# Kernel tuning notes

Measured on AMD Instinct MI355X. Metric: run time of the kernel, lower is better.

The kernel has to match this reference:

```python
import jax, jax.numpy as jnp
import numpy as np

N, E, IN, H, L = 50000, 640000, 64, 128, 3
EPS_DIST = 1e-8
LN_EPS = 1e-5


def setup_inputs() -> dict:
    key = jax.random.key(0)
    ks = iter(jax.random.split(key, 64))

    def rn(shape, fan_in):
        return (jax.random.normal(next(ks), shape, jnp.float32) / np.sqrt(fan_in)).astype(jnp.float32)

    inp = {}
    inp['h'] = jax.random.normal(next(ks), (N, IN), jnp.float32)
    inp['x'] = jax.random.normal(next(ks), (N, 3), jnp.float32)
    inp['edge_index'] = jax.random.randint(next(ks), (2, E), 0, N, jnp.int64)
    # embedding_in: Linear(IN, H)
    inp['W_emb'] = rn((IN, H), IN); inp['b_emb'] = jnp.zeros((H,), jnp.float32)
    # per-layer EquivariantConv params, stacked over L
    inp['Wm1'] = rn((L, 2 * H + 1, H), 2 * H + 1); inp['bm1'] = jnp.zeros((L, H), jnp.float32)
    inp['Wm2'] = rn((L, H, H), H);                 inp['bm2'] = jnp.zeros((L, H), jnp.float32)
    inp['Wc1'] = rn((L, H, H), H);                 inp['bc1'] = jnp.zeros((L, H), jnp.float32)
    inp['Wc2'] = rn((L, H, 1), H)  # no bias
    inp['Wn1'] = rn((L, 2 * H, H), 2 * H);         inp['bn1'] = jnp.zeros((L, H), jnp.float32)
    inp['Wn2'] = rn((L, H, H), H);                 inp['bn2'] = jnp.zeros((L, H), jnp.float32)
    inp['ln_g'] = jnp.ones((L, H), jnp.float32);   inp['ln_b'] = jnp.zeros((L, H), jnp.float32)
    # epsilon head params
    inp['Wem1'] = rn((2 * H + 4, H), 2 * H + 4);   inp['bem1'] = jnp.zeros((H,), jnp.float32)
    inp['Wem2'] = rn((H, H), H);                   inp['bem2'] = jnp.zeros((H,), jnp.float32)
    inp['Wec1'] = rn((H, H), H);                   inp['bec1'] = jnp.zeros((H,), jnp.float32)
    inp['Wec2'] = rn((H, 3), H);                   inp['bec2'] = jnp.zeros((3,), jnp.float32)
    inp['Wh1'] = rn((H + 3, H), H + 3);            inp['bh1'] = jnp.zeros((H,), jnp.float32)
    inp['Wh2'] = rn((H, 3), H);                    inp['bh2'] = jnp.zeros((3,), jnp.float32)
    return inp


def _layernorm(v, g, b):
    mu = jnp.mean(v, axis=-1, keepdims=True)
    var = jnp.mean((v - mu) ** 2, axis=-1, keepdims=True)
    return (v - mu) * jax.lax.rsqrt(var + LN_EPS) * g + b


def reference(h, x, edge_index, W_emb, b_emb, Wm1, bm1, Wm2, bm2, Wc1, bc1, Wc2,
              Wn1, bn1, Wn2, bn2, ln_g, ln_b, Wem1, bem1, Wem2, bem2,
              Wec1, bec1, Wec2, bec2, Wh1, bh1, Wh2, bh2):
    row, col = edge_index[0], edge_index[1]
    n = x.shape[0]
    seg = lambda v: jax.ops.segment_sum(v, col, num_segments=n)
    in_degree = seg(jnp.ones((col.shape[0], 1), x.dtype))  # [N,1]

    h = h @ W_emb + b_emb  # embedding_in

    for i in range(L):
        rel = x[row] - x[col]                                   # [E,3]
        dist = jnp.linalg.norm(rel, axis=-1, keepdims=True)     # [E,1]
        mi = jnp.concatenate([h[row], h[col], dist], axis=-1)   # [E,2H+1]
        m = jax.nn.silu(jax.nn.silu(mi @ Wm1[i] + bm1[i]) @ Wm2[i] + bm2[i])
        agg = seg(m)                                            # [N,H]
        rel_dir = rel / (dist + EPS_DIST)
        coord_mult = jnp.tanh(jax.nn.silu(m @ Wc1[i] + bc1[i]) @ Wc2[i])  # [E,1]
        coord_update = seg(coord_mult * rel_dir)                # [N,3]
        x = x + coord_update / (in_degree + 1.0)
        nu = jnp.concatenate([h, agg], axis=-1)
        h = h + jax.nn.silu(nu @ Wn1[i] + bn1[i]) @ Wn2[i] + bn2[i]
        h = _layernorm(h, ln_g[i], ln_b[i])

    # predict_epsilon (eps_directional_head=False, eps_use_local_head=True, eps_normalize_agg=False)
    rel = x[row] - x[col]
    dist = jnp.linalg.norm(rel, axis=-1, keepdims=True)
    mi = jnp.concatenate([h[row], h[col], rel, dist], axis=-1)  # [E,2H+4]
    em = jax.nn.silu(jax.nn.silu(mi @ Wem1 + bem1) @ Wem2 + bem2)
    eps_src = jax.nn.silu(em @ Wec1 + bec1) @ Wec2 + bec2       # [E,3]
    eps = seg(eps_src)                                          # [N,3]
    hx = jnp.concatenate([h, x], axis=-1)
    eps = eps + jax.nn.silu(hx @ Wh1 + bh1) @ Wh2 + bh2
    return (h, x, eps)
```

## Files before the change

kernel.cpp:

```cpp
#include <hip/hip_runtime.h>

#define N_NODES 50000
#define N_EDGES 640000
#define HDIM    128
#define NLAYERS 3

typedef __attribute__((ext_vector_type(4))) float f32x4;
typedef short s16x8 __attribute__((ext_vector_type(8)));
typedef __bf16 bf16v8 __attribute__((ext_vector_type(8)));

static __device__ __forceinline__ unsigned short f2b(float f){
  unsigned int u = __float_as_uint(f);
  unsigned int r = u + 0x7FFFu + ((u >> 16) & 1u);
  return (unsigned short)(r >> 16);
}
static __device__ __forceinline__ float b2f(unsigned short h){
  return __uint_as_float(((unsigned int)h) << 16);
}
static __device__ __forceinline__ float silu_f(float x){
  return x / (1.0f + __expf(-x));
}
static __device__ __forceinline__ f32x4 MFMA(s16x8 a, s16x8 b, f32x4 c){
  return __builtin_amdgcn_mfma_f32_16x16x32_bf16(
      __builtin_bit_cast(bf16v8, a), __builtin_bit_cast(bf16v8, b), c, 0, 0, 0);
}

static __device__ __forceinline__ s16x8 ldA(const unsigned short* __restrict__ WT,
                                            int K, int s, int kk, int lane){
  const unsigned short* p = WT + (size_t)((s<<4) + (lane&15))*K + (kk<<5) + ((lane>>4)<<2);
  ushort4 a = *(const ushort4*)p;
  ushort4 b = *(const ushort4*)(p + 16);
  s16x8 r;
  r[0]=(short)a.x; r[1]=(short)a.y; r[2]=(short)a.z; r[3]=(short)a.w;
  r[4]=(short)b.x; r[5]=(short)b.y; r[6]=(short)b.z; r[7]=(short)b.w;
  return r;
}
static __device__ __forceinline__ s16x8 ldBf32(const float* __restrict__ p, int q){
  float4 a = *(const float4*)(p + (q<<2));
  float4 b = *(const float4*)(p + 16 + (q<<2));
  s16x8 r;
  r[0]=(short)f2b(a.x); r[1]=(short)f2b(a.y); r[2]=(short)f2b(a.z); r[3]=(short)f2b(a.w);
  r[4]=(short)f2b(b.x); r[5]=(short)f2b(b.y); r[6]=(short)f2b(b.z); r[7]=(short)f2b(b.w);
  return r;
}

#define STAGE(T) do { \
    const unsigned short* _src = blob + (((size_t)(T))<<12) + (w<<10) + (lane<<3); \
    unsigned char* _dst = &sm.wbuf[(T)&1][w<<11]; \
    __builtin_amdgcn_global_load_lds((const __attribute__((address_space(1))) void*)_src, \
        (__attribute__((address_space(3))) void*)_dst, 16, 0, 0); \
    __builtin_amdgcn_global_load_lds((const __attribute__((address_space(1))) void*)(_src+512), \
        (__attribute__((address_space(3))) void*)(_dst+1024), 16, 0, 0); \
  } while(0)
#define WAITV2 asm volatile("s_waitcnt vmcnt(2)" ::: "memory")
#define WAITV0 asm volatile("s_waitcnt vmcnt(0)" ::: "memory")
#define BARF do{ __builtin_amdgcn_s_barrier(); asm volatile("" ::: "memory"); }while(0)
#define EBAR do{ asm volatile("" ::: "memory"); __builtin_amdgcn_s_barrier(); }while(0)

__global__ void k_conv(const float* __restrict__ W, unsigned short* __restrict__ WT, int kshift){
  const int K = 1 << kshift;
  const int idx = (blockIdx.x<<8) + threadIdx.x;
  if (idx < (K<<7)){
    const int n = idx >> kshift;
    const int k = idx & (K-1);
    WT[idx] = f2b(W[(size_t)k*HDIM + n]);
  }
}

__global__ void k_conv_blob(const float* __restrict__ W1, const float* __restrict__ W2,
                            const float* __restrict__ W3, unsigned short* __restrict__ blob){
  const int i = (blockIdx.x<<8) + threadIdx.x;
  const int t = i >> 12;
  const int n = (i >> 5) & 127;
  const int slot = (i >> 3) & 3;
  const int j = i & 7;
  const int q = slot ^ ((n >> 1) & 3);
  const int kl = ((j >> 2) << 4) + (q << 2) + (j & 3);
  const float* W; int k;
  if (t < 8){ W = W1; k = (t<<5) + kl; }
  else if (t < 12){ W = W2; k = ((t-8)<<5) + kl; }
  else { W = W3; k = ((t-12)<<5) + kl; }
  blob[i] = f2b(W[(size_t)k*HDIM + n]);
}

__global__ void k_degree(const int* __restrict__ coli, int* __restrict__ degi){
  const int e = (blockIdx.x<<8) + threadIdx.x;
  if (e < N_EDGES) atomicAdd(&degi[coli[e]], 1);
}
__global__ void k_scanA(const int* __restrict__ degi, int* __restrict__ off, int* __restrict__ bsum){
  const int t = threadIdx.x, b = blockIdx.x;
  const int i = (b<<8) + t;
  const int v = (i < N_NODES) ? degi[i] : 0;
  int x = v;
  const int lane = t & 63;
  #pragma unroll
  for (int d=1; d<64; d<<=1){ int y = __shfl_up(x, d); if (lane >= d) x += y; }
  __shared__ int wsum[4];
  if (lane == 63) wsum[t>>6] = x;
  __syncthreads();
  int wo = 0;
  #pragma unroll
  for (int w=0; w<4; ++w) if (w < (t>>6)) wo += wsum[w];
  const int incl = x + wo;
  if (i < N_NODES) off[i] = incl - v;
  if (t == 255) bsum[b] = incl;
}
__global__ void k_scanB(int* __restrict__ bsum, int nb){
  const int t = threadIdx.x;
  const int v = (t < nb) ? bsum[t] : 0;
  int x = v;
  const int lane = t & 63;
  #pragma unroll
  for (int d=1; d<64; d<<=1){ int y = __shfl_up(x, d); if (lane >= d) x += y; }
  __shared__ int wsum[4];
  if (lane == 63) wsum[t>>6] = x;
  __syncthreads();
  int wo = 0;
  #pragma unroll
  for (int w=0; w<4; ++w) if (w < (t>>6)) wo += wsum[w];
  const int incl = x + wo;
  if (t < nb) bsum[t] = incl - v;
}
__global__ void k_scanC(int* __restrict__ off, const int* __restrict__ bsum, int* __restrict__ cursor){
  const int i = (blockIdx.x<<8) + threadIdx.x;
  if (i < N_NODES){
    const int o = off[i] + bsum[i>>8];
    off[i] = o;
    cursor[i] = o;
  }
}
__global__ void k_fill(const int* __restrict__ coli, int* __restrict__ cursor, int* __restrict__ elist){
  const int e = (blockIdx.x<<8) + threadIdx.x;
  if (e < N_EDGES){
    const int p = atomicAdd(&cursor[coli[e]], 1);
    elist[p] = e;
  }
}
__global__ void k_xcopy(const float* __restrict__ xin, float* __restrict__ xbuf){
  const int i = (blockIdx.x<<8) + threadIdx.x;
  if (i < N_NODES*3) xbuf[i] = xin[i];
}

__global__ __launch_bounds__(256) void k_embed(
    const float* __restrict__ hin, const unsigned short* __restrict__ WembT,
    const float* __restrict__ bemb, float* __restrict__ hbuf,
    unsigned short* __restrict__ hb)
{
  __shared__ float s_b[128];
  const int tid = threadIdx.x;
  if (tid < 128) s_b[tid] = bemb[tid];
  __syncthreads();
  const int lane = tid & 63, q = lane>>4;
  const int n = (blockIdx.x<<6) + ((tid>>6)<<4) + (lane&15);
  const bool valid = n < N_NODES;
  const int nc = valid ? n : (N_NODES-1);
  const float* __restrict__ hp = hin + (size_t)nc*64;
  f32x4 acc[8];
  #pragma unroll
  for (int s=0;s<8;++s)
    #pragma unroll
    for (int r=0;r<4;++r) acc[s][r] = s_b[(s<<4)+(q<<2)+r];
  #pragma unroll
  for (int kk=0;kk<2;++kk){
    const s16x8 bf = ldBf32(hp + (kk<<5), q);
    #pragma unroll
    for (int s=0;s<8;++s) acc[s] = MFMA(ldA(WembT, 64, s, kk, lane), bf, acc[s]);
  }
  if (valid){
    float* op = hbuf + (size_t)n*HDIM;
    unsigned short* hbw = hb + (size_t)n*HDIM;
    #pragma unroll
    for (int s=0;s<8;++s){
      float4 o; o.x=acc[s][0]; o.y=acc[s][1]; o.z=acc[s][2]; o.w=acc[s][3];
      *(float4*)(op + (s<<4) + (q<<2)) = o;
      ushort4 u; u.x=f2b(o.x); u.y=f2b(o.y); u.z=f2b(o.z); u.w=f2b(o.w);
      *(ushort4*)(hbw + ((s>>1)<<5) + (q<<3) + ((s&1)<<2)) = u;
    }
  }
}

template<bool CSR>
__global__ __launch_bounds__(256) void k_edge_mlp(
    const unsigned short* __restrict__ hb, const float* __restrict__ xbuf,
    const int* __restrict__ rowi, const int* __restrict__ coli,
    const unsigned short* __restrict__ blob,
    const float* __restrict__ bm1v, const float* __restrict__ wm1r256,
    const float* __restrict__ bm2v, const float* __restrict__ bc1v,
    const float* __restrict__ wc2v,
    unsigned short* __restrict__ m_buf, float* __restrict__ agg,
    float* __restrict__ cu)
{
  __shared__ struct {
    alignas(16) unsigned char wbuf[2][8192];
    int row[128]; int col[128];
    float dist[128]; float rdir[128][3];
    float b1[128], w256[128], b2[128], bc1[128], wc2[128];
  } sm;
  const int tid = threadIdx.x;
  const int ebase = blockIdx.x << 7;
  const int lane = tid & 63, w = tid >> 6, q = lane >> 4;
  if (tid < 128){
    const int e = ebase + tid;
    const int r = rowi[e], c = coli[e];
    sm.row[tid] = r; sm.col[tid] = c;
    const float dx = xbuf[3*r+0] - xbuf[3*c+0];
    const float dy = xbuf[3*r+1] - xbuf[3*c+1];
    const float dz = xbuf[3*r+2] - xbuf[3*c+2];
    const float d = sqrtf(dx*dx + dy*dy + dz*dz);
    sm.dist[tid] = d;
    const float inv = 1.0f / (d + 1e-8f);
    sm.rdir[tid][0] = dx*inv; sm.rdir[tid][1] = dy*inv; sm.rdir[tid][2] = dz*inv;
  } else {
    const int f = tid - 128;
    sm.b1[f] = bm1v[f]; sm.w256[f] = wm1r256[f]; sm.b2[f] = bm2v[f];
    sm.bc1[f] = bc1v[f]; sm.wc2[f] = wc2v[f];
  }
  STAGE(0);
  __syncthreads();

  const int toff = ((lane&15)<<6) + ((q ^ ((lane>>1)&3))<<4);
  const int q8 = q << 3;
  const int el0 = (w<<5) + (lane&15);
  const int el1 = el0 + 16;
  const unsigned short* __restrict__ hr0 = hb + (size_t)sm.row[el0]*HDIM;
  const unsigned short* __restrict__ hc0 = hb + (size_t)sm.col[el0]*HDIM;
  const unsigned short* __restrict__ hr1 = hb + (size_t)sm.row[el1]*HDIM;
  const unsigned short* __restrict__ hc1 = hb + (size_t)sm.col[el1]*HDIM;
  const float d0 = sm.dist[el0], d1 = sm.dist[el1];

  f32x4 acc0[8], acc1[8];
  #pragma unroll
  for (int s=0;s<8;++s)
    #pragma unroll
    for (int r=0;r<4;++r){
      const int f = (s<<4)+(q<<2)+r;
      acc0[s][r] = sm.b1[f] + d0 * sm.w256[f];
      acc1[s][r] = sm.b1[f] + d1 * sm.w256[f];
    }
  s16x8 B0 = *(const s16x8*)(hr0 + q8);
  s16x8 B1 = *(const s16x8*)(hr1 + q8);
  #pragma unroll
  for (int t=0;t<8;++t){
    STAGE(t+1);
    WAITV2; BARF;
    s16x8 nB0, nB1;
    if (t < 7){
      const int kk = t+1;
      const int ho = ((kk&3)<<5) + q8;
      nB0 = *(const s16x8*)(((kk<4)?hr0:hc0) + ho);
      nB1 = *(const s16x8*)(((kk<4)?hr1:hc1) + ho);
    }
    #pragma unroll
    for (int s=0;s<8;++s){
      const s16x8 A = *(const s16x8*)(&sm.wbuf[t&1][(s<<10)+toff]);
      acc0[s] = MFMA(A, B0, acc0[s]);
      acc1[s] = MFMA(A, B1, acc1[s]);
    }
    EBAR;
    if (t < 7){ B0 = nB0; B1 = nB1; }
  }

  s16x8 sb0[4], sb1[4];
  #pragma unroll
  for (int t=0;t<4;++t)
    #pragma unroll
    for (int j=0;j<8;++j){
      sb0[t][j] = (short)f2b(silu_f(acc0[(t<<1)+(j>>2)][j&3]));
      sb1[t][j] = (short)f2b(silu_f(acc1[(t<<1)+(j>>2)][j&3]));
    }

  f32x4 acc20[8], acc21[8];
  #pragma unroll
  for (int s=0;s<8;++s)
    #pragma unroll
    for (int r=0;r<4;++r){
      const float b = sm.b2[(s<<4)+(q<<2)+r];
      acc20[s][r] = b; acc21[s][r] = b;
    }
  #pragma unroll
  for (int t=0;t<4;++t){
    STAGE(9+t);
    WAITV2; BARF;
    #pragma unroll
    for (int s=0;s<8;++s){
      const s16x8 A = *(const s16x8*)(&sm.wbuf[t&1][(s<<10)+toff]);
      acc20[s] = MFMA(A, sb0[t], acc20[s]);
      acc21[s] = MFMA(A, sb1[t], acc21[s]);
    }
    EBAR;
  }
  s16x8 mb0[4], mb1[4];
  #pragma unroll
  for (int t=0;t<4;++t)
    #pragma unroll
    for (int j=0;j<8;++j){
      mb0[t][j] = (short)f2b(silu_f(acc20[(t<<1)+(j>>2)][j&3]));
      mb1[t][j] = (short)f2b(silu_f(acc21[(t<<1)+(j>>2)][j&3]));
    }

  f32x4 acc30[8], acc31[8];
  #pragma unroll
  for (int s=0;s<8;++s)
    #pragma unroll
    for (int r=0;r<4;++r){
      const float b = sm.bc1[(s<<4)+(q<<2)+r];
      acc30[s][r] = b; acc31[s][r] = b;
    }
  #pragma unroll
  for (int t=0;t<4;++t){
    if (t < 3){ STAGE(13+t); WAITV2; } else { WAITV0; }
    BARF;
    #pragma unroll
    for (int s=0;s<8;++s){
      const s16x8 A = *(const s16x8*)(&sm.wbuf[t&1][(s<<10)+toff]);
      acc30[s] = MFMA(A, mb0[t], acc30[s]);
      acc31[s] = MFMA(A, mb1[t], acc31[s]);
    }
    EBAR;
  }

  float dot0 = 0.f, dot1 = 0.f;
  #pragma unroll
  for (int s=0;s<8;++s)
    #pragma unroll
    for (int r=0;r<4;++r){
      const int f = (s<<4)+(q<<2)+r;
      dot0 += silu_f(acc30[s][r]) * sm.wc2[f];
      dot1 += silu_f(acc31[s][r]) * sm.wc2[f];
    }
  dot0 += __shfl_xor(dot0, 16); dot0 += __shfl_xor(dot0, 32);
  dot1 += __shfl_xor(dot1, 16); dot1 += __shfl_xor(dot1, 32);
  const float cm0 = tanhf(dot0), cm1 = tanhf(dot1);
  if (q < 3){
    atomicAdd(&cu[(size_t)sm.col[el0]*3 + q], cm0 * sm.rdir[el0][q]);
    atomicAdd(&cu[(size_t)sm.col[el1]*3 + q], cm1 * sm.rdir[el1][q]);
  }
  if (CSR){
    unsigned short* mp0 = m_buf + (size_t)(ebase+el0)*HDIM + q8;
    unsigned short* mp1 = m_buf + (size_t)(ebase+el1)*HDIM + q8;
    #pragma unroll
    for (int t=0;t<4;++t){
      *(s16x8*)(mp0 + (t<<5)) = mb0[t];
      *(s16x8*)(mp1 + (t<<5)) = mb1[t];
    }
  } else {
    float* ap0 = agg + (size_t)sm.col[el0]*HDIM + (q<<2);
    float* ap1 = agg + (size_t)sm.col[el1]*HDIM + (q<<2);
    #pragma unroll
    for (int t=0;t<4;++t)
      #pragma unroll
      for (int j=0;j<8;++j){
        const int o = (((t<<1)+(j>>2))<<4) + (j&3);
        atomicAdd(ap0 + o, b2f((unsigned short)mb0[t][j]));
        atomicAdd(ap1 + o, b2f((unsigned short)mb1[t][j]));
      }
  }
}

template<bool CSR>
__global__ __launch_bounds__(256) void k_node_mlp(
    float* __restrict__ hbuf, unsigned short* __restrict__ hb,
    float* __restrict__ xbuf,
    const unsigned short* __restrict__ m_buf, const float* __restrict__ agg,
    const int* __restrict__ off, const int* __restrict__ degi, const int* __restrict__ elist,
    const float* __restrict__ cu,
    const unsigned short* __restrict__ Wn1T, const float* __restrict__ bn1v,
    const unsigned short* __restrict__ Wn2T, const float* __restrict__ bn2v,
    const float* __restrict__ lng, const float* __restrict__ lnb)
{
  __shared__ float s_bn1[128], s_bn2[128], s_g[128], s_b[128];
  const int tid = threadIdx.x;
  const int nbase = blockIdx.x << 6;
  if (tid >= 128){
    const int f = tid - 128;
    s_bn1[f]=bn1v[f]; s_bn2[f]=bn2v[f]; s_g[f]=lng[f]; s_b[f]=lnb[f];
  } else if (tid < 64){
    const int n = nbase + tid;
    if (n < N_NODES){
      const float dd = (float)degi[n] + 1.0f;
      #pragma unroll
      for (int c=0;c<3;++c) xbuf[3*n+c] += cu[3*n+c] / dd;
    }
  }
  __syncthreads();

  const int lane = tid & 63, q = lane >> 4;
  const int q8 = q << 3;
  const int n = nbase + ((tid>>6)<<4) + (lane & 15);
  const bool valid = (n < N_NODES);
  const int nc = valid ? n : (N_NODES-1);
  const float* __restrict__ hp = hbuf + (size_t)nc*HDIM;
  const unsigned short* __restrict__ hbp = hb + (size_t)nc*HDIM;

  float aggv[4][8];
  #pragma unroll
  for (int kk=0;kk<4;++kk)
    #pragma unroll
    for (int j=0;j<8;++j) aggv[kk][j]=0.f;
  if (CSR){
    const int st = off[nc];
    const int cnt = degi[nc];
    for (int ii=0; ii<cnt; ++ii){
      const unsigned short* mrow = m_buf + (size_t)elist[st+ii]*HDIM;
      #pragma unroll
      for (int kk=0;kk<4;++kk){
        const s16x8 v = *(const s16x8*)(mrow + (kk<<5) + q8);
        #pragma unroll
        for (int j=0;j<8;++j) aggv[kk][j] += b2f((unsigned short)v[j]);
      }
    }
  } else {
    const float* ap = agg + (size_t)nc*HDIM;
    #pragma unroll
    for (int kk=0;kk<4;++kk){
      float4 a = *(const float4*)(ap + (kk<<5) + (q<<2));
      float4 b = *(const float4*)(ap + (kk<<5) + 16 + (q<<2));
      aggv[kk][0]=a.x; aggv[kk][1]=a.y; aggv[kk][2]=a.z; aggv[kk][3]=a.w;
      aggv[kk][4]=b.x; aggv[kk][5]=b.y; aggv[kk][6]=b.z; aggv[kk][7]=b.w;
    }
  }

  f32x4 acc[8];
  #pragma unroll
  for (int s=0;s<8;++s)
    #pragma unroll
    for (int r=0;r<4;++r) acc[s][r] = s_bn1[(s<<4)+(q<<2)+r];
  #pragma unroll
  for (int kk=0;kk<4;++kk){
    const s16x8 bf = *(const s16x8*)(hbp + (kk<<5) + q8);
    #pragma unroll
    for (int s=0;s<8;++s) acc[s] = MFMA(ldA(Wn1T, 256, s, kk, lane), bf, acc[s]);
  }
  #pragma unroll
  for (int kk=0;kk<4;++kk){
    s16x8 bf;
    #pragma unroll
    for (int j=0;j<8;++j) bf[j] = (short)f2b(aggv[kk][j]);
    #pragma unroll
    for (int s=0;s<8;++s) acc[s] = MFMA(ldA(Wn1T, 256, s, kk+4, lane), bf, acc[s]);
  }
  s16x8 sb[4];
  #pragma unroll
  for (int t=0;t<4;++t)
    #pragma unroll
    for (int j=0;j<8;++j)
      sb[t][j] = (short)f2b(silu_f(acc[(t<<1)+(j>>2)][j&3]));
  f32x4 acc2[8];
  #pragma unroll
  for (int s=0;s<8;++s)
    #pragma unroll
    for (int r=0;r<4;++r) acc2[s][r] = s_bn2[(s<<4)+(q<<2)+r];
  #pragma unroll
  for (int kk=0;kk<4;++kk){
    #pragma unroll
    for (int s=0;s<8;++s) acc2[s] = MFMA(ldA(Wn2T, 128, s, kk, lane), sb[kk], acc2[s]);
  }

  float v[8][4];
  float sum = 0.f;
  #pragma unroll
  for (int s=0;s<8;++s){
    float4 h4 = *(const float4*)(hp + (s<<4) + (q<<2));
    v[s][0] = h4.x + acc2[s][0]; v[s][1] = h4.y + acc2[s][1];
    v[s][2] = h4.z + acc2[s][2]; v[s][3] = h4.w + acc2[s][3];
    sum += v[s][0]+v[s][1]+v[s][2]+v[s][3];
  }
  sum += __shfl_xor(sum, 16);
  sum += __shfl_xor(sum, 32);
  const float mu = sum * (1.0f/128.0f);
  float vs = 0.f;
  #pragma unroll
  for (int s=0;s<8;++s)
    #pragma unroll
    for (int r=0;r<4;++r){ const float d = v[s][r]-mu; vs += d*d; }
  vs += __shfl_xor(vs, 16);
  vs += __shfl_xor(vs, 32);
  const float rs = rsqrtf(vs*(1.0f/128.0f) + 1e-5f);
  if (valid){
    float* op = hbuf + (size_t)n*HDIM;
    unsigned short* hbw = hb + (size_t)n*HDIM;
    #pragma unroll
    for (int s=0;s<8;++s){
      const int f0 = (s<<4)+(q<<2);
      float4 o;
      o.x = (v[s][0]-mu)*rs*s_g[f0+0] + s_b[f0+0];
      o.y = (v[s][1]-mu)*rs*s_g[f0+1] + s_b[f0+1];
      o.z = (v[s][2]-mu)*rs*s_g[f0+2] + s_b[f0+2];
      o.w = (v[s][3]-mu)*rs*s_g[f0+3] + s_b[f0+3];
      *(float4*)(op + f0) = o;
      ushort4 u; u.x=f2b(o.x); u.y=f2b(o.y); u.z=f2b(o.z); u.w=f2b(o.w);
      *(ushort4*)(hbw + ((s>>1)<<5) + q8 + ((s&1)<<2)) = u;
    }
  }
}

__global__ __launch_bounds__(256) void k_eps_edge(
    const unsigned short* __restrict__ hb, const float* __restrict__ xbuf,
    const int* __restrict__ rowi, const int* __restrict__ coli,
    const unsigned short* __restrict__ blob,
    const float* __restrict__ bem1v, const float* __restrict__ wem_rows,
    const float* __restrict__ bem2v, const float* __restrict__ bec1v,
    const float* __restrict__ Wec2, const float* __restrict__ bec2,
    float* __restrict__ epsb)
{
  __shared__ struct {
    alignas(16) unsigned char wbuf[2][8192];
    int row[128]; int col[128];
    float rel[128][3]; float dist[128];
    float b1[128], w4[4][128], b2[128], bc1[128], wc[3][128];
  } sm;
  const int tid = threadIdx.x;
  const int ebase = blockIdx.x << 7;
  const int lane = tid & 63, w = tid >> 6, q = lane >> 4;
  if (tid < 128){
    const int e = ebase + tid;
    const int r = rowi[e], c = coli[e];
    sm.row[tid]=r; sm.col[tid]=c;
    const float dx = xbuf[3*r+0]-xbuf[3*c+0];
    const float dy = xbuf[3*r+1]-xbuf[3*c+1];
    const float dz = xbuf[3*r+2]-xbuf[3*c+2];
    sm.rel[tid][0]=dx; sm.rel[tid][1]=dy; sm.rel[tid][2]=dz;
    sm.dist[tid] = sqrtf(dx*dx+dy*dy+dz*dz);
  } else {
    const int f = tid - 128;
    sm.b1[f]=bem1v[f];
    sm.w4[0][f]=wem_rows[f];     sm.w4[1][f]=wem_rows[128+f];
    sm.w4[2][f]=wem_rows[256+f]; sm.w4[3][f]=wem_rows[384+f];
    sm.b2[f]=bem2v[f]; sm.bc1[f]=bec1v[f];
    sm.wc[0][f]=Wec2[f*3+0]; sm.wc[1][f]=Wec2[f*3+1]; sm.wc[2][f]=Wec2[f*3+2];
  }
  STAGE(0);
  __syncthreads();

  const int toff = ((lane&15)<<6) + ((q ^ ((lane>>1)&3))<<4);
  const int q8 = q << 3;
  const int el0 = (w<<5) + (lane&15);
  const int el1 = el0 + 16;
  const unsigned short* __restrict__ hr0 = hb + (size_t)sm.row[el0]*HDIM;
  const unsigned short* __restrict__ hc0 = hb + (size_t)sm.col[el0]*HDIM;
  const unsigned short* __restrict__ hr1 = hb + (size_t)sm.row[el1]*HDIM;
  const unsigned short* __restrict__ hc1 = hb + (size_t)sm.col[el1]*HDIM;
  const float r00=sm.rel[el0][0], r01=sm.rel[el0][1], r02=sm.rel[el0][2], d0=sm.dist[el0];
  const float r10=sm.rel[el1][0], r11=sm.rel[el1][1], r12=sm.rel[el1][2], d1=sm.dist[el1];

  f32x4 acc0[8], acc1[8];
  #pragma unroll
  for (int s=0;s<8;++s)
    #pragma unroll
    for (int r=0;r<4;++r){
      const int f = (s<<4)+(q<<2)+r;
      acc0[s][r] = sm.b1[f] + r00*sm.w4[0][f] + r01*sm.w4[1][f] + r02*sm.w4[2][f] + d0*sm.w4[3][f];
      acc1[s][r] = sm.b1[f] + r10*sm.w4[0][f] + r11*sm.w4[1][f] + r12*sm.w4[2][f] + d1*sm.w4[3][f];
    }
  s16x8 B0 = *(const s16x8*)(hr0 + q8);
  s16x8 B1 = *(const s16x8*)(hr1 + q8);
  #pragma unroll
  for (int t=0;t<8;++t){
    STAGE(t+1);
    WAITV2; BARF;
    s16x8 nB0, nB1;
    if (t < 7){
      const int kk = t+1;
      const int ho = ((kk&3)<<5) + q8;
      nB0 = *(const s16x8*)(((kk<4)?hr0:hc0) + ho);
      nB1 = *(const s16x8*)(((kk<4)?hr1:hc1) + ho);
    }
    #pragma unroll
    for (int s=0;s<8;++s){
      const s16x8 A = *(const s16x8*)(&sm.wbuf[t&1][(s<<10)+toff]);
      acc0[s] = MFMA(A, B0, acc0[s]);
      acc1[s] = MFMA(A, B1, acc1[s]);
    }
    EBAR;
    if (t < 7){ B0 = nB0; B1 = nB1; }
  }

  s16x8 sb0[4], sb1[4];
  #pragma unroll
  for (int t=0;t<4;++t)
    #pragma unroll
    for (int j=0;j<8;++j){
      sb0[t][j] = (short)f2b(silu_f(acc0[(t<<1)+(j>>2)][j&3]));
      sb1[t][j] = (short)f2b(silu_f(acc1[(t<<1)+(j>>2)][j&3]));
    }
  f32x4 acc20[8], acc21[8];
  #pragma unroll
  for (int s=0;s<8;++s)
    #pragma unroll
    for (int r=0;r<4;++r){
      const float b = sm.b2[(s<<4)+(q<<2)+r];
      acc20[s][r] = b; acc21[s][r] = b;
    }
  #pragma unroll
  for (int t=0;t<4;++t){
    STAGE(9+t);
    WAITV2; BARF;
    #pragma unroll
    for (int s=0;s<8;++s){
      const s16x8 A = *(const s16x8*)(&sm.wbuf[t&1][(s<<10)+toff]);
      acc20[s] = MFMA(A, sb0[t], acc20[s]);
      acc21[s] = MFMA(A, sb1[t], acc21[s]);
    }
    EBAR;
  }
  s16x8 mb0[4], mb1[4];
  #pragma unroll
  for (int t=0;t<4;++t)
    #pragma unroll
    for (int j=0;j<8;++j){
      mb0[t][j] = (short)f2b(silu_f(acc20[(t<<1)+(j>>2)][j&3]));
      mb1[t][j] = (short)f2b(silu_f(acc21[(t<<1)+(j>>2)][j&3]));
    }
  f32x4 acc30[8], acc31[8];
  #pragma unroll
  for (int s=0;s<8;++s)
    #pragma unroll
    for (int r=0;r<4;++r){
      const float b = sm.bc1[(s<<4)+(q<<2)+r];
      acc30[s][r] = b; acc31[s][r] = b;
    }
  #pragma unroll
  for (int t=0;t<4;++t){
    if (t < 3){ STAGE(13+t); WAITV2; } else { WAITV0; }
    BARF;
    #pragma unroll
    for (int s=0;s<8;++s){
      const s16x8 A = *(const s16x8*)(&sm.wbuf[t&1][(s<<10)+toff]);
      acc30[s] = MFMA(A, mb0[t], acc30[s]);
      acc31[s] = MFMA(A, mb1[t], acc31[s]);
    }
    EBAR;
  }

  float e00=0.f,e01=0.f,e02=0.f, e10=0.f,e11=0.f,e12=0.f;
  #pragma unroll
  for (int s=0;s<8;++s)
    #pragma unroll
    for (int r=0;r<4;++r){
      const int f = (s<<4)+(q<<2)+r;
      const float ev0 = silu_f(acc30[s][r]);
      const float ev1 = silu_f(acc31[s][r]);
      e00 += ev0*sm.wc[0][f]; e01 += ev0*sm.wc[1][f]; e02 += ev0*sm.wc[2][f];
      e10 += ev1*sm.wc[0][f]; e11 += ev1*sm.wc[1][f]; e12 += ev1*sm.wc[2][f];
    }
  e00 += __shfl_xor(e00,16); e00 += __shfl_xor(e00,32);
  e01 += __shfl_xor(e01,16); e01 += __shfl_xor(e01,32);
  e02 += __shfl_xor(e02,16); e02 += __shfl_xor(e02,32);
  e10 += __shfl_xor(e10,16); e10 += __shfl_xor(e10,32);
  e11 += __shfl_xor(e11,16); e11 += __shfl_xor(e11,32);
  e12 += __shfl_xor(e12,16); e12 += __shfl_xor(e12,32);
  if (q < 3){
    const float v0 = (q==0)?e00:((q==1)?e01:e02);
    const float v1 = (q==0)?e10:((q==1)?e11:e12);
    const float bq = bec2[q];
    atomicAdd(&epsb[(size_t)sm.col[el0]*3 + q], v0 + bq);
    atomicAdd(&epsb[(size_t)sm.col[el1]*3 + q], v1 + bq);
  }
}

__global__ __launch_bounds__(256) void k_eps_node(
    const float* __restrict__ hbuf, const float* __restrict__ xbuf,
    const unsigned short* __restrict__ Wh1T, const float* __restrict__ bh1v,
    const float* __restrict__ wh1_rows,
    const float* __restrict__ Wh2, const float* __restrict__ bh2,
    float* __restrict__ epsb)
{
  __shared__ float s_bh1[128], s_w3[3][128], s_wc[3][128];
  const int tid = threadIdx.x;
  if (tid >= 128){
    const int f = tid - 128;
    s_bh1[f]=bh1v[f];
    s_w3[0][f]=wh1_rows[f]; s_w3[1][f]=wh1_rows[128+f]; s_w3[2][f]=wh1_rows[256+f];
    s_wc[0][f]=Wh2[f*3+0]; s_wc[1][f]=Wh2[f*3+1]; s_wc[2][f]=Wh2[f*3+2];
  }
  __syncthreads();
  const int lane = tid & 63, q = lane >> 4;
  const int n = (blockIdx.x<<6) + ((tid>>6)<<4) + (lane & 15);
  const bool valid = n < N_NODES;
  const int nc = valid ? n : (N_NODES-1);
  const float* __restrict__ hp = hbuf + (size_t)nc*HDIM;
  const float x0 = xbuf[3*nc+0], x1 = xbuf[3*nc+1], x2 = xbuf[3*nc+2];
  f32x4 acc[8];
  #pragma unroll
  for (int s=0;s<8;++s)
    #pragma unroll
    for (int r=0;r<4;++r){
      const int f = (s<<4)+(q<<2)+r;
      acc[s][r] = s_bh1[f] + x0*s_w3[0][f] + x1*s_w3[1][f] + x2*s_w3[2][f];
    }
  #pragma unroll
  for (int kk=0;kk<4;++kk){
    const s16x8 bf = ldBf32(hp + (kk<<5), q);
    #pragma unroll
    for (int s=0;s<8;++s) acc[s] = MFMA(ldA(Wh1T, 128, s, kk, lane), bf, acc[s]);
  }
  float d0=0.f, d1=0.f, d2=0.f;
  #pragma unroll
  for (int s=0;s<8;++s)
    #pragma unroll
    for (int r=0;r<4;++r){
      const int f = (s<<4)+(q<<2)+r;
      const float ev = silu_f(acc[s][r]);
      d0 += ev*s_wc[0][f]; d1 += ev*s_wc[1][f]; d2 += ev*s_wc[2][f];
    }
  d0 += __shfl_xor(d0,16); d0 += __shfl_xor(d0,32);
  d1 += __shfl_xor(d1,16); d1 += __shfl_xor(d1,32);
  d2 += __shfl_xor(d2,16); d2 += __shfl_xor(d2,32);
  if (valid && q < 3){
    const float val = (q==0)?d0:((q==1)?d1:d2);
    epsb[(size_t)n*3 + q] += val + bh2[q];
  }
}

extern "C" void kernel_launch(void* const* d_in, const int* in_sizes, int n_in,
                              void* d_out, int out_size, void* d_ws, size_t ws_size,
                              hipStream_t stream)
{
  (void)in_sizes; (void)n_in; (void)out_size;
  const float* h_in  = (const float*)d_in[0];
  const float* x_in  = (const float*)d_in[1];
  const int*   eidx  = (const int*)d_in[2];
  const float* W_emb = (const float*)d_in[3];
  const float* b_emb = (const float*)d_in[4];
  const float* Wm1 = (const float*)d_in[5];
  const float* bm1 = (const float*)d_in[6];
  const float* Wm2 = (const float*)d_in[7];
  const float* bm2 = (const float*)d_in[8];
  const float* Wc1 = (const float*)d_in[9];
  const float* bc1 = (const float*)d_in[10];
  const float* Wc2 = (const float*)d_in[11];
  const float* Wn1 = (const float*)d_in[12];
  const float* bn1 = (const float*)d_in[13];
  const float* Wn2 = (const float*)d_in[14];
  const float* bn2 = (const float*)d_in[15];
  const float* lng = (const float*)d_in[16];
  const float* lnb = (const float*)d_in[17];
  const float* Wem1 = (const float*)d_in[18];
  const float* bem1 = (const float*)d_in[19];
  const float* Wem2 = (const float*)d_in[20];
  const float* bem2 = (const float*)d_in[21];
  const float* Wec1 = (const float*)d_in[22];
  const float* bec1 = (const float*)d_in[23];
  const float* Wec2 = (const float*)d_in[24];
  const float* bec2 = (const float*)d_in[25];
  const float* Wh1 = (const float*)d_in[26];
  const float* bh1 = (const float*)d_in[27];
  const float* Wh2 = (const float*)d_in[28];
  const float* bh2 = (const float*)d_in[29];

  const int* rowi = eidx;
  const int* coli = eidx + N_EDGES;

  float* hbuf = (float*)d_out;
  float* xbuf = hbuf + (size_t)N_NODES*HDIM;
  float* epsb = xbuf + (size_t)N_NODES*3;

  char* wp = (char*)d_ws;
  auto alloc = [&](size_t bytes)->char*{
    char* p = wp; wp += (bytes + 255) & ~(size_t)255; return p;
  };
  unsigned short* WembT = (unsigned short*)alloc((size_t)128*64*2);
  unsigned short *Wn1T[NLAYERS], *Wn2T[NLAYERS];
  for (int i=0;i<NLAYERS;++i){
    Wn1T[i] = (unsigned short*)alloc((size_t)128*256*2);
    Wn2T[i] = (unsigned short*)alloc((size_t)128*128*2);
  }
  unsigned short* Wh1T  = (unsigned short*)alloc((size_t)128*128*2);
  unsigned short* blobL = (unsigned short*)alloc((size_t)NLAYERS*65536*2);
  unsigned short* blobE = (unsigned short*)alloc((size_t)65536*2);
  unsigned short* hb    = (unsigned short*)alloc((size_t)N_NODES*HDIM*2);
  int* degi   = (int*)alloc((size_t)N_NODES*4);
  int* offv   = (int*)alloc((size_t)N_NODES*4);
  int* cursor = (int*)alloc((size_t)N_NODES*4);
  int* bsum   = (int*)alloc(4096);
  float* cu   = (float*)alloc((size_t)N_NODES*3*4);
  int* elist  = (int*)alloc((size_t)N_EDGES*4);
  char* big   = alloc((size_t)N_EDGES*HDIM*2);
  const bool use_csr = ((size_t)(wp - (char*)d_ws) <= ws_size);
  unsigned short* m_buf = (unsigned short*)big;
  float* agg = (float*)big;

  auto conv = [&](const float* W, unsigned short* WT, int kshift){
    const int tot = 128 << kshift;
    k_conv<<<dim3((tot+255)/256), dim3(256), 0, stream>>>(W, WT, kshift);
  };
  conv(W_emb, WembT, 6);
  for (int i=0;i<NLAYERS;++i){
    conv(Wn1 + (size_t)i*256*128, Wn1T[i], 8);
    conv(Wn2 + (size_t)i*128*128, Wn2T[i], 7);
  }
  conv(Wh1,  Wh1T,  7);
  for (int i=0;i<NLAYERS;++i)
    k_conv_blob<<<dim3(256), dim3(256), 0, stream>>>(
        Wm1 + (size_t)i*257*128, Wm2 + (size_t)i*128*128, Wc1 + (size_t)i*128*128,
        blobL + (size_t)i*65536);
  k_conv_blob<<<dim3(256), dim3(256), 0, stream>>>(Wem1, Wem2, Wec1, blobE);

  hipMemsetAsync(degi, 0, (size_t)N_NODES*4, stream);
  k_degree<<<dim3((N_EDGES+255)/256), dim3(256), 0, stream>>>(coli, degi);
  const int nb = (N_NODES + 255)/256;
  if (use_csr){
    k_scanA<<<dim3(nb), dim3(256), 0, stream>>>(degi, offv, bsum);
    k_scanB<<<dim3(1), dim3(256), 0, stream>>>(bsum, nb);
    k_scanC<<<dim3(nb), dim3(256), 0, stream>>>(offv, bsum, cursor);
    k_fill<<<dim3((N_EDGES+255)/256), dim3(256), 0, stream>>>(coli, cursor, elist);
  }
  k_xcopy<<<dim3((N_NODES*3+255)/256), dim3(256), 0, stream>>>(x_in, xbuf);
  k_embed<<<dim3((N_NODES+63)/64), dim3(256), 0, stream>>>(h_in, WembT, b_emb, hbuf, hb);

  for (int i=0;i<NLAYERS;++i){
    hipMemsetAsync(cu, 0, (size_t)N_NODES*3*4, stream);
    if (!use_csr) hipMemsetAsync(agg, 0, (size_t)N_NODES*HDIM*4, stream);
    const float* wm1r256 = Wm1 + (size_t)i*257*128 + (size_t)256*128;
    if (use_csr){
      k_edge_mlp<true><<<dim3(N_EDGES/128), dim3(256), 0, stream>>>(
        hb, xbuf, rowi, coli, blobL + (size_t)i*65536,
        bm1 + i*128, wm1r256, bm2 + i*128, bc1 + i*128, Wc2 + i*128,
        m_buf, agg, cu);
      k_node_mlp<true><<<dim3((N_NODES+63)/64), dim3(256), 0, stream>>>(
        hbuf, hb, xbuf, m_buf, agg, offv, degi, elist, cu,
        Wn1T[i], bn1 + i*128, Wn2T[i], bn2 + i*128, lng + i*128, lnb + i*128);
    } else {
      k_edge_mlp<false><<<dim3(N_EDGES/128), dim3(256), 0, stream>>>(
        hb, xbuf, rowi, coli, blobL + (size_t)i*65536,
        bm1 + i*128, wm1r256, bm2 + i*128, bc1 + i*128, Wc2 + i*128,
        m_buf, agg, cu);
      k_node_mlp<false><<<dim3((N_NODES+63)/64), dim3(256), 0, stream>>>(
        hbuf, hb, xbuf, m_buf, agg, offv, degi, elist, cu,
        Wn1T[i], bn1 + i*128, Wn2T[i], bn2 + i*128, lng + i*128, lnb + i*128);
    }
  }
  hipMemsetAsync(epsb, 0, (size_t)N_NODES*3*4, stream);
  k_eps_edge<<<dim3(N_EDGES/128), dim3(256), 0, stream>>>(
    hb, xbuf, rowi, coli, blobE,
    bem1, Wem1 + (size_t)256*128, bem2, bec1, Wec2, bec2, epsb);
  k_eps_node<<<dim3((N_NODES+63)/64), dim3(256), 0, stream>>>(
    hbuf, xbuf, Wh1T, bh1, Wh1 + (size_t)128*128, Wh2, bh2, epsb);
}
```

Measured before the change: 1.382 ms.

## Widen edge MLP tiles to 256 edges and scatter messages into CSR order

The edge MLP and epsilon edge kernels now process 256 edges per block (64 per wave), so each staged weight tile in LDS is reused by four 16-edge groups instead of two. The tiles are staged in double-width chunks. The bias and distance/rel terms are folded into an extra K-tile of the weight blob, fed by a constant-1 input column. Messages are written directly to their CSR-sorted slot through a permutation, so the node kernel reads them contiguously instead of through an indirection list. Packed bf16 conversion instructions are also added. The trade-off is higher register pressure (launch_bounds 256,2) and larger LDS use, which may reduce occupancy.

```diff
diff --git a/kernel.cpp b/kernel.cpp
--- a/kernel.cpp
+++ b/kernel.cpp
@@ -19,6 +19,19 @@
 }
 static __device__ __forceinline__ float silu_f(float x){
   return x / (1.0f + __expf(-x));
+}
+static __device__ __forceinline__ unsigned int cvt2(float a, float b){
+  unsigned int r;
+  asm("v_cvt_pk_bf16_f32 %0, %1, %2" : "=v"(r) : "v"(a), "v"(b));
+  return r;
+}
+static __device__ __forceinline__ s16x8 siluPack(const f32x4 a, const f32x4 b){
+  union { unsigned int u[4]; s16x8 v; } r;
+  r.u[0] = cvt2(silu_f(a[0]), silu_f(a[1]));
+  r.u[1] = cvt2(silu_f(a[2]), silu_f(a[3]));
+  r.u[2] = cvt2(silu_f(b[0]), silu_f(b[1]));
+  r.u[3] = cvt2(silu_f(b[2]), silu_f(b[3]));
+  return r.v;
 }
 static __device__ __forceinline__ f32x4 MFMA(s16x8 a, s16x8 b, f32x4 c){
   return __builtin_amdgcn_mfma_f32_16x16x32_bf16(
@@ -44,18 +57,34 @@
   return r;
 }
 
-#define STAGE(T) do { \
-    const unsigned short* _src = blob + (((size_t)(T))<<12) + (w<<10) + (lane<<3); \
-    unsigned char* _dst = &sm.wbuf[(T)&1][w<<11]; \
-    __builtin_amdgcn_global_load_lds((const __attribute__((address_space(1))) void*)_src, \
-        (__attribute__((address_space(3))) void*)_dst, 16, 0, 0); \
-    __builtin_amdgcn_global_load_lds((const __attribute__((address_space(1))) void*)(_src+512), \
-        (__attribute__((address_space(3))) void*)(_dst+1024), 16, 0, 0); \
-  } while(0)
-#define WAITV2 asm volatile("s_waitcnt vmcnt(2)" ::: "memory")
-#define WAITV0 asm volatile("s_waitcnt vmcnt(0)" ::: "memory")
+#define GLL(SRC, DST) __builtin_amdgcn_global_load_lds( \
+    (const __attribute__((address_space(1))) void*)(SRC), \
+    (__attribute__((address_space(3))) void*)(DST), 16, 0, 0)
+#define STG2(T0,BUF) do{ \
+    const unsigned short* _s = blob + (((size_t)(T0))<<12) + (w<<11) + (lane<<3); \
+    unsigned char* _d = &sm.wbuf[BUF][(w<<12) + (lane<<4)]; \
+    GLL(_s, _d); GLL(_s+512, _d+1024); GLL(_s+1024, _d+2048); GLL(_s+1536, _d+3072); \
+  }while(0)
+#define STG1(T0,BUF) do{ \
+    const unsigned short* _s = blob + (((size_t)(T0))<<12) + (w<<10) + (lane<<3); \
+    unsigned char* _d = &sm.wbuf[BUF][(w<<11) + (lane<<4)]; \
+    GLL(_s, _d); GLL(_s+512, _d+1024); \
+  }while(0)
+#define WAITV(N) asm volatile("s_waitcnt vmcnt(" #N ")" ::: "memory")
 #define BARF do{ __builtin_amdgcn_s_barrier(); asm volatile("" ::: "memory"); }while(0)
 #define EBAR do{ asm volatile("" ::: "memory"); __builtin_amdgcn_s_barrier(); }while(0)
+
+#define PH2(BUF, BEXPR, ACC) do{ \
+  _Pragma("unroll") for (int ti=0; ti<2; ++ti){ \
+    _Pragma("unroll") for (int s=0;s<8;++s){ \
+      const s16x8 _A = *(const s16x8*)&sm.wbuf[BUF][(ti<<13)+(s<<10)+toff]; \
+      _Pragma("unroll") for (int e=0;e<4;++e) ACC[e][s] = MFMA(_A, (BEXPR), ACC[e][s]); \
+    } } }while(0)
+#define PH1(BUF, BEXPR, ACC) do{ \
+  _Pragma("unroll") for (int s=0;s<8;++s){ \
+    const s16x8 _A = *(const s16x8*)&sm.wbuf[BUF][(s<<10)+toff]; \
+    _Pragma("unroll") for (int e=0;e<4;++e) ACC[e][s] = MFMA(_A, (BEXPR), ACC[e][s]); \
+  } }while(0)
 
 __global__ void k_conv(const float* __restrict__ W, unsigned short* __restrict__ WT, int kshift){
   const int K = 1 << kshift;
@@ -68,19 +97,23 @@
 }
 
 __global__ void k_conv_blob(const float* __restrict__ W1, const float* __restrict__ W2,
-                            const float* __restrict__ W3, unsigned short* __restrict__ blob){
+                            const float* __restrict__ W3, const float* __restrict__ aux,
+                            const float* __restrict__ bias, int naux,
+                            unsigned short* __restrict__ blob){
   const int i = (blockIdx.x<<8) + threadIdx.x;
+  if (i >= 17*4096) return;
   const int t = i >> 12;
   const int n = (i >> 5) & 127;
   const int slot = (i >> 3) & 3;
   const int j = i & 7;
   const int q = slot ^ ((n >> 1) & 3);
   const int kl = ((j >> 2) << 4) + (q << 2) + (j & 3);
-  const float* W; int k;
-  if (t < 8){ W = W1; k = (t<<5) + kl; }
-  else if (t < 12){ W = W2; k = ((t-8)<<5) + kl; }
-  else { W = W3; k = ((t-12)<<5) + kl; }
-  blob[i] = f2b(W[(size_t)k*HDIM + n]);
+  float v;
+  if (t == 0)      v = (kl < naux) ? aux[(size_t)kl*HDIM + n] : (kl == 16 ? bias[n] : 0.f);
+  else if (t < 9)  v = W1[(size_t)(((t-1)<<5)+kl)*HDIM + n];
+  else if (t < 13) v = W2[(size_t)(((t-9)<<5)+kl)*HDIM + n];
+  else             v = W3[(size_t)(((t-13)<<5)+kl)*HDIM + n];
+  blob[i] = f2b(v);
 }
 
 __global__ void k_degree(const int* __restrict__ coli, int* __restrict__ degi){
@@ -129,11 +162,11 @@
     cursor[i] = o;
   }
 }
-__global__ void k_fill(const int* __restrict__ coli, int* __restrict__ cursor, int* __restrict__ elist){
+__global__ void k_fill(const int* __restrict__ coli, int* __restrict__ cursor, int* __restrict__ perm){
   const int e = (blockIdx.x<<8) + threadIdx.x;
   if (e < N_EDGES){
     const int p = atomicAdd(&cursor[coli[e]], 1);
-    elist[p] = e;
+    perm[e] = p;
   }
 }
 __global__ void k_xcopy(const float* __restrict__ xin, float* __restrict__ xbuf){
@@ -180,29 +213,29 @@
 }
 
 template<bool CSR>
-__global__ __launch_bounds__(256) void k_edge_mlp(
+__global__ __launch_bounds__(256,2) void k_edge_mlp(
     const unsigned short* __restrict__ hb, const float* __restrict__ xbuf,
     const int* __restrict__ rowi, const int* __restrict__ coli,
-    const unsigned short* __restrict__ blob,
-    const float* __restrict__ bm1v, const float* __restrict__ wm1r256,
+    const int* __restrict__ perm, const unsigned short* __restrict__ blob,
     const float* __restrict__ bm2v, const float* __restrict__ bc1v,
     const float* __restrict__ wc2v,
     unsigned short* __restrict__ m_buf, float* __restrict__ agg,
     float* __restrict__ cu)
 {
   __shared__ struct {
-    alignas(16) unsigned char wbuf[2][8192];
-    int row[128]; int col[128];
-    float dist[128]; float rdir[128][3];
-    float b1[128], w256[128], b2[128], bc1[128], wc2[128];
+    alignas(16) unsigned char wbuf[2][16384];
+    int row[256], col[256], prm[256];
+    float dist[256]; float rdir[256][3];
+    float b2[128], bc1[128], wc2[128];
   } sm;
-  const int tid = threadIdx.x;
-  const int ebase = blockIdx.x << 7;
-  const int lane = tid & 63, w = tid >> 6, q = lane >> 4;
-  if (tid < 128){
+  const int tid = threadIdx.x, lane = tid & 63, w = tid >> 6, q = lane >> 4;
+  const int q8 = q << 3;
+  const int ebase = blockIdx.x << 8;
+  {
     const int e = ebase + tid;
     const int r = rowi[e], c = coli[e];
     sm.row[tid] = r; sm.col[tid] = c;
+    if (CSR) sm.prm[tid] = perm[e];
     const float dx = xbuf[3*r+0] - xbuf[3*c+0];
     const float dy = xbuf[3*r+1] - xbuf[3*c+1];
     const float dz = xbuf[3*r+2] - xbuf[3*c+2];
@@ -210,150 +243,137 @@
     sm.dist[tid] = d;
     const float inv = 1.0f / (d + 1e-8f);
     sm.rdir[tid][0] = dx*inv; sm.rdir[tid][1] = dy*inv; sm.rdir[tid][2] = dz*inv;
+  }
+  if (tid < 128){ sm.b2[tid]=bm2v[tid]; sm.bc1[tid]=bc1v[tid]; sm.wc2[tid]=wc2v[tid]; }
+  STG2(0,0); STG2(2,1);
+  __syncthreads();
+
+  const int toff = ((lane&15)<<6) + ((q ^ ((lane>>1)&3))<<4);
+  int rn[4], cn[4];
+  #pragma unroll
+  for (int e=0;e<4;++e){
+    const int el = (w<<6) + (e<<4) + (lane&15);
+    rn[e] = sm.row[el]; cn[e] = sm.col[el];
+  }
+  s16x8 BA[4][2], BB[4][2];
+  #pragma unroll
+  for (int e=0;e<4;++e){
+    const int el = (w<<6) + (e<<4) + (lane&15);
+    s16x8 bx = {0,0,0,0,0,0,0,0};
+    if (q == 0){ bx[0] = (short)f2b(sm.dist[el]); bx[4] = (short)0x3F80; }
+    BA[e][0] = bx;
+    BA[e][1] = *(const s16x8*)(hb + ((size_t)rn[e]<<7) + q8);
+  }
+  f32x4 acc[4][8] = {};
+
+  BARF;
+  #pragma unroll
+  for (int e=0;e<4;++e){
+    BB[e][0] = *(const s16x8*)(hb + ((size_t)rn[e]<<7) + 32 + q8);
+    BB[e][1] = *(const s16x8*)(hb + ((size_t)rn[e]<<7) + 64 + q8);
+  }
+  PH2(0, BA[e][ti], acc);
+  EBAR; STG2(4,0);
+  BARF;
+  #pragma unroll
+  for (int e=0;e<4;++e){
+    BA[e][0] = *(const s16x8*)(hb + ((size_t)rn[e]<<7) + 96 + q8);
+    BA[e][1] = *(const s16x8*)(hb + ((size_t)cn[e]<<7) + q8);
+  }
+  PH2(1, BB[e][ti], acc);
+  EBAR; STG2(6,1);
+  WAITV(12); BARF;
+  #pragma unroll
+  for (int e=0;e<4;++e){
+    BB[e][0] = *(const s16x8*)(hb + ((size_t)cn[e]<<7) + 32 + q8);
+    BB[e][1] = *(const s16x8*)(hb + ((size_t)cn[e]<<7) + 64 + q8);
+  }
+  PH2(0, BA[e][ti], acc);
+  EBAR; STG1(8,0);
+  WAITV(10); BARF;
+  #pragma unroll
+  for (int e=0;e<4;++e)
+    BA[e][0] = *(const s16x8*)(hb + ((size_t)cn[e]<<7) + 96 + q8);
+  PH2(1, BB[e][ti], acc);
+  EBAR; STG2(9,1);
+  WAITV(8); BARF;
+  PH1(0, BA[e][0], acc);
+  EBAR; STG2(11,0);
+
+  s16x8 sb[4][4];
+  #pragma unroll
+  for (int e=0;e<4;++e)
+    #pragma unroll
+    for (int c=0;c<4;++c) sb[e][c] = siluPack(acc[e][2*c], acc[e][2*c+1]);
+  f32x4 acc2[4][8];
+  #pragma unroll
+  for (int s=0;s<8;++s){
+    const f32x4 b = *(const f32x4*)&sm.b2[(s<<4)+(q<<2)];
+    #pragma unroll
+    for (int e=0;e<4;++e) acc2[e][s] = b;
+  }
+  WAITV(4); BARF;
+  PH2(1, sb[e][ti], acc2);
+  EBAR; STG2(13,1);
+  WAITV(4); BARF;
+  PH2(0, sb[e][2+ti], acc2);
+  EBAR; STG2(15,0);
+
+  s16x8 mb[4][4];
+  #pragma unroll
+  for (int e=0;e<4;++e)
+    #pragma unroll
+    for (int c=0;c<4;++c) mb[e][c] = siluPack(acc2[e][2*c], acc2[e][2*c+1]);
+  f32x4 acc3[4][8];
+  #pragma unroll
+  for (int s=0;s<8;++s){
+    const f32x4 b = *(const f32x4*)&sm.bc1[(s<<4)+(q<<2)];
+    #pragma unroll
+    for (int e=0;e<4;++e) acc3[e][s] = b;
+  }
+  WAITV(4); BARF;
+  PH2(1, mb[e][ti], acc3);
+  EBAR;
+  WAITV(0); BARF;
+  PH2(0, mb[e][2+ti], acc3);
+
+  float dot[4] = {0.f,0.f,0.f,0.f};
+  #pragma unroll
+  for (int s=0;s<8;++s){
+    const f32x4 wv = *(const f32x4*)&sm.wc2[(s<<4)+(q<<2)];
+    #pragma unroll
+    for (int e=0;e<4;++e)
+      #pragma unroll
+      for (int r=0;r<4;++r) dot[e] += silu_f(acc3[e][s][r]) * wv[r];
+  }
+  #pragma unroll
+  for (int e=0;e<4;++e){
+    dot[e] += __shfl_xor(dot[e], 16);
+    dot[e] += __shfl_xor(dot[e], 32);
+    const float cm = tanhf(dot[e]);
+    const int el = (w<<6) + (e<<4) + (lane&15);
+    if (q < 3) atomicAdd(&cu[(size_t)cn[e]*3 + q], cm * sm.rdir[el][q]);
+  }
+  if (CSR){
+    #pragma unroll
+    for (int e=0;e<4;++e){
+      const int el = (w<<6) + (e<<4) + (lane&15);
+      unsigned short* mp = m_buf + ((size_t)sm.prm[el]<<7) + q8;
+      #pragma unroll
+      for (int c=0;c<4;++c) *(s16x8*)(mp + (c<<5)) = mb[e][c];
+    }
   } else {
-    const int f = tid - 128;
-    sm.b1[f] = bm1v[f]; sm.w256[f] = wm1r256[f]; sm.b2[f] = bm2v[f];
-    sm.bc1[f] = bc1v[f]; sm.wc2[f] = wc2v[f];
-  }
-  STAGE(0);
-  __syncthreads();
-
-  const int toff = ((lane&15)<<6) + ((q ^ ((lane>>1)&3))<<4);
-  const int q8 = q << 3;
-  const int el0 = (w<<5) + (lane&15);
-  const int el1 = el0 + 16;
-  const unsigned short* __restrict__ hr0 = hb + (size_t)sm.row[el0]*HDIM;
-  const unsigned short* __restrict__ hc0 = hb + (size_t)sm.col[el0]*HDIM;
-  const unsigned short* __restrict__ hr1 = hb + (size_t)sm.row[el1]*HDIM;
-  const unsigned short* __restrict__ hc1 = hb + (size_t)sm.col[el1]*HDIM;
-  const float d0 = sm.dist[el0], d1 = sm.dist[el1];
-
-  f32x4 acc0[8], acc1[8];
-  #pragma unroll
-  for (int s=0;s<8;++s)
-    #pragma unroll
-    for (int r=0;r<4;++r){
-      const int f = (s<<4)+(q<<2)+r;
-      acc0[s][r] = sm.b1[f] + d0 * sm.w256[f];
-      acc1[s][r] = sm.b1[f] + d1 * sm.w256[f];
-    }
-  s16x8 B0 = *(const s16x8*)(hr0 + q8);
-  s16x8 B1 = *(const s16x8*)(hr1 + q8);
-  #pragma unroll
-  for (int t=0;t<8;++t){
-    STAGE(t+1);
-    WAITV2; BARF;
-    s16x8 nB0, nB1;
-    if (t < 7){
-      const int kk = t+1;
-      const int ho = ((kk&3)<<5) + q8;
-      nB0 = *(const s16x8*)(((kk<4)?hr0:hc0) + ho);
-      nB1 = *(const s16x8*)(((kk<4)?hr1:hc1) + ho);
-    }
-    #pragma unroll
-    for (int s=0;s<8;++s){
-      const s16x8 A = *(const s16x8*)(&sm.wbuf[t&1][(s<<10)+toff]);
-      acc0[s] = MFMA(A, B0, acc0[s]);
-      acc1[s] = MFMA(A, B1, acc1[s]);
-    }
-    EBAR;
-    if (t < 7){ B0 = nB0; B1 = nB1; }
-  }
-
-  s16x8 sb0[4], sb1[4];
-  #pragma unroll
-  for (int t=0;t<4;++t)
-    #pragma unroll
-    for (int j=0;j<8;++j){
-      sb0[t][j] = (short)f2b(silu_f(acc0[(t<<1)+(j>>2)][j&3]));
-      sb1[t][j] = (short)f2b(silu_f(acc1[(t<<1)+(j>>2)][j&3]));
-    }
-
-  f32x4 acc20[8], acc21[8];
-  #pragma unroll
-  for (int s=0;s<8;++s)
-    #pragma unroll
-    for (int r=0;r<4;++r){
-      const float b = sm.b2[(s<<4)+(q<<2)+r];
-      acc20[s][r] = b; acc21[s][r] = b;
-    }
-  #pragma unroll
-  for (int t=0;t<4;++t){
-    STAGE(9+t);
-    WAITV2; BARF;
-    #pragma unroll
-    for (int s=0;s<8;++s){
-      const s16x8 A = *(const s16x8*)(&sm.wbuf[t&1][(s<<10)+toff]);
-      acc20[s] = MFMA(A, sb0[t], acc20[s]);
-      acc21[s] = MFMA(A, sb1[t], acc21[s]);
-    }
-    EBAR;
-  }
-  s16x8 mb0[4], mb1[4];
-  #pragma unroll
-  for (int t=0;t<4;++t)
-    #pragma unroll
-    for (int j=0;j<8;++j){
-      mb0[t][j] = (short)f2b(silu_f(acc20[(t<<1)+(j>>2)][j&3]));
-      mb1[t][j] = (short)f2b(silu_f(acc21[(t<<1)+(j>>2)][j&3]));
-    }
-
-  f32x4 acc30[8], acc31[8];
-  #pragma unroll
-  for (int s=0;s<8;++s)
-    #pragma unroll
-    for (int r=0;r<4;++r){
-      const float b = sm.bc1[(s<<4)+(q<<2)+r];
-      acc30[s][r] = b; acc31[s][r] = b;
-    }
-  #pragma unroll
-  for (int t=0;t<4;++t){
-    if (t < 3){ STAGE(13+t); WAITV2; } else { WAITV0; }
-    BARF;
-    #pragma unroll
-    for (int s=0;s<8;++s){
-      const s16x8 A = *(const s16x8*)(&sm.wbuf[t&1][(s<<10)+toff]);
-      acc30[s] = MFMA(A, mb0[t], acc30[s]);
-      acc31[s] = MFMA(A, mb1[t], acc31[s]);
-    }
-    EBAR;
-  }
-
-  float dot0 = 0.f, dot1 = 0.f;
-  #pragma unroll
-  for (int s=0;s<8;++s)
-    #pragma unroll
-    for (int r=0;r<4;++r){
-      const int f = (s<<4)+(q<<2)+r;
-      dot0 += silu_f(acc30[s][r]) * sm.wc2[f];
-      dot1 += silu_f(acc31[s][r]) * sm.wc2[f];
-    }
-  dot0 += __shfl_xor(dot0, 16); dot0 += __shfl_xor(dot0, 32);
-  dot1 += __shfl_xor(dot1, 16); dot1 += __shfl_xor(dot1, 32);
-  const float cm0 = tanhf(dot0), cm1 = tanhf(dot1);
-  if (q < 3){
-    atomicAdd(&cu[(size_t)sm.col[el0]*3 + q], cm0 * sm.rdir[el0][q]);
-    atomicAdd(&cu[(size_t)sm.col[el1]*3 + q], cm1 * sm.rdir[el1][q]);
-  }
-  if (CSR){
-    unsigned short* mp0 = m_buf + (size_t)(ebase+el0)*HDIM + q8;
-    unsigned short* mp1 = m_buf + (size_t)(ebase+el1)*HDIM + q8;
-    #pragma unroll
-    for (int t=0;t<4;++t){
-      *(s16x8*)(mp0 + (t<<5)) = mb0[t];
-      *(s16x8*)(mp1 + (t<<5)) = mb1[t];
-    }
-  } else {
-    float* ap0 = agg + (size_t)sm.col[el0]*HDIM + (q<<2);
-    float* ap1 = agg + (size_t)sm.col[el1]*HDIM + (q<<2);
-    #pragma unroll
-    for (int t=0;t<4;++t)
+    #pragma unroll
+    for (int e=0;e<4;++e){
+      float* ap = agg + (size_t)cn[e]*HDIM + (q<<2);
       #pragma unroll
-      for (int j=0;j<8;++j){
-        const int o = (((t<<1)+(j>>2))<<4) + (j&3);
-        atomicAdd(ap0 + o, b2f((unsigned short)mb0[t][j]));
-        atomicAdd(ap1 + o, b2f((unsigned short)mb1[t][j]));
-      }
+      for (int c=0;c<4;++c)
+        #pragma unroll
+        for (int j=0;j<8;++j){
+          const int o = (((c<<1)+(j>>2))<<4) + (j&3);
+          atomicAdd(ap + o, b2f((unsigned short)mb[e][c][j]));
+        }
+    }
   }
 }
 
@@ -362,7 +382,7 @@
     float* __restrict__ hbuf, unsigned short* __restrict__ hb,
     float* __restrict__ xbuf,
     const unsigned short* __restrict__ m_buf, const float* __restrict__ agg,
-    const int* __restrict__ off, const int* __restrict__ degi, const int* __restrict__ elist,
+    const int* __restrict__ off, const int* __restrict__ degi,
     const float* __restrict__ cu,
     const unsigned short* __restrict__ Wn1T, const float* __restrict__ bn1v,
     const unsigned short* __restrict__ Wn2T, const float* __restrict__ bn2v,
@@ -401,7 +421,7 @@
     const int st = off[nc];
     const int cnt = degi[nc];
     for (int ii=0; ii<cnt; ++ii){
-      const unsigned short* mrow = m_buf + (size_t)elist[st+ii]*HDIM;
+      const unsigned short* mrow = m_buf + ((size_t)(st+ii)<<7);
       #pragma unroll
       for (int kk=0;kk<4;++kk){
         const s16x8 v = *(const s16x8*)(mrow + (kk<<5) + q8);
@@ -494,25 +514,24 @@
   }
 }
 
-__global__ __launch_bounds__(256) void k_eps_edge(
+__global__ __launch_bounds__(256,2) void k_eps_edge(
     const unsigned short* __restrict__ hb, const float* __restrict__ xbuf,
     const int* __restrict__ rowi, const int* __restrict__ coli,
     const unsigned short* __restrict__ blob,
-    const float* __restrict__ bem1v, const float* __restrict__ wem_rows,
     const float* __restrict__ bem2v, const float* __restrict__ bec1v,
     const float* __restrict__ Wec2, const float* __restrict__ bec2,
     float* __restrict__ epsb)
 {
   __shared__ struct {
-    alignas(16) unsigned char wbuf[2][8192];
-    int row[128]; int col[128];
-    float rel[128][3]; float dist[128];
-    float b1[128], w4[4][128], b2[128], bc1[128], wc[3][128];
+    alignas(16) unsigned char wbuf[2][16384];
+    int row[256], col[256];
+    float rel[256][3]; float dist[256];
+    float b2[128], bc1[128], wc[3][128];
   } sm;
-  const int tid = threadIdx.x;
-  const int ebase = blockIdx.x << 7;
-  const int lane = tid & 63, w = tid >> 6, q = lane >> 4;
-  if (tid < 128){
+  const int tid = threadIdx.x, lane = tid & 63, w = tid >> 6, q = lane >> 4;
+  const int q8 = q << 3;
+  const int ebase = blockIdx.x << 8;
+  {
     const int e = ebase + tid;
     const int r = rowi[e], c = coli[e];
     sm.row[tid]=r; sm.col[tid]=c;
@@ -521,140 +540,132 @@
     const float dz = xbuf[3*r+2]-xbuf[3*c+2];
     sm.rel[tid][0]=dx; sm.rel[tid][1]=dy; sm.rel[tid][2]=dz;
     sm.dist[tid] = sqrtf(dx*dx+dy*dy+dz*dz);
-  } else {
-    const int f = tid - 128;
-    sm.b1[f]=bem1v[f];
-    sm.w4[0][f]=wem_rows[f];     sm.w4[1][f]=wem_rows[128+f];
-    sm.w4[2][f]=wem_rows[256+f]; sm.w4[3][f]=wem_rows[384+f];
-    sm.b2[f]=bem2v[f]; sm.bc1[f]=bec1v[f];
-    sm.wc[0][f]=Wec2[f*3+0]; sm.wc[1][f]=Wec2[f*3+1]; sm.wc[2][f]=Wec2[f*3+2];
-  }
-  STAGE(0);
+  }
+  if (tid < 128){
+    sm.b2[tid]=bem2v[tid]; sm.bc1[tid]=bec1v[tid];
+    sm.wc[0][tid]=Wec2[tid*3+0]; sm.wc[1][tid]=Wec2[tid*3+1]; sm.wc[2][tid]=Wec2[tid*3+2];
+  }
+  STG2(0,0); STG2(2,1);
   __syncthreads();
 
   const int toff = ((lane&15)<<6) + ((q ^ ((lane>>1)&3))<<4);
-  const int q8 = q << 3;
-  const int el0 = (w<<5) + (lane&15);
-  const int el1 = el0 + 16;
-  const unsigned short* __restrict__ hr0 = hb + (size_t)sm.row[el0]*HDIM;
-  const unsigned short* __restrict__ hc0 = hb + (size_t)sm.col[el0]*HDIM;
-  const unsigned short* __restrict__ hr1 = hb + (size_t)sm.row[el1]*HDIM;
-  const unsigned short* __restrict__ hc1 = hb + (size_t)sm.col[el1]*HDIM;
-  const float r00=sm.rel[el0][0], r01=sm.rel[el0][1], r02=sm.rel[el0][2], d0=sm.dist[el0];
-  const float r10=sm.rel[el1][0], r11=sm.rel[el1][1], r12=sm.rel[el1][2], d1=sm.dist[el1];
-
-  f32x4 acc0[8], acc1[8];
-  #pragma unroll
-  for (int s=0;s<8;++s)
-    #pragma unroll
-    for (int r=0;r<4;++r){
-      const int f = (s<<4)+(q<<2)+r;
-      acc0[s][r] = sm.b1[f] + r00*sm.w4[0][f] + r01*sm.w4[1][f] + r02*sm.w4[2][f] + d0*sm.w4[3][f];
-      acc1[s][r] = sm.b1[f] + r10*sm.w4[0][f] + r11*sm.w4[1][f] + r12*sm.w4[2][f] + d1*sm.w4[3][f];
-    }
-  s16x8 B0 = *(const s16x8*)(hr0 + q8);
-  s16x8 B1 = *(const s16x8*)(hr1 + q8);
-  #pragma unroll
-  for (int t=0;t<8;++t){
-    STAGE(t+1);
-    WAITV2; BARF;
-    s16x8 nB0, nB1;
-    if (t < 7){
-      const int kk = t+1;
-      const int ho = ((kk&3)<<5) + q8;
-      nB0 = *(const s16x8*)(((kk<4)?hr0:hc0) + ho);
-      nB1 = *(const s16x8*)(((kk<4)?hr1:hc1) + ho);
-    }
-    #pragma unroll
-    for (int s=0;s<8;++s){
-      const s16x8 A = *(const s16x8*)(&sm.wbuf[t&1][(s<<10)+toff]);
-      acc0[s] = MFMA(A, B0, acc0[s]);
-      acc1[s] = MFMA(A, B1, acc1[s]);
-    }
-    EBAR;
-    if (t < 7){ B0 = nB0; B1 = nB1; }
-  }
-
-  s16x8 sb0[4], sb1[4];
-  #pragma unroll
-  for (int t=0;t<4;++t)
-    #pragma unroll
-    for (int j=0;j<8;++j){
-      sb0[t][j] = (short)f2b(silu_f(acc0[(t<<1)+(j>>2)][j&3]));
-      sb1[t][j] = (short)f2b(silu_f(acc1[(t<<1)+(j>>2)][j&3]));
-    }
-  f32x4 acc20[8], acc21[8];
-  #pragma unroll
-  for (int s=0;s<8;++s)
-    #pragma unroll
-    for (int r=0;r<4;++r){
-      const float b = sm.b2[(s<<4)+(q<<2)+r];
-      acc20[s][r] = b; acc21[s][r] = b;
-    }
-  #pragma unroll
-  for (int t=0;t<4;++t){
-    STAGE(9+t);
-    WAITV2; BARF;
-    #pragma unroll
-    for (int s=0;s<8;++s){
-      const s16x8 A = *(const s16x8*)(&sm.wbuf[t&1][(s<<10)+toff]);
-      acc20[s] = MFMA(A, sb0[t], acc20[s]);
-      acc21[s] = MFMA(A, sb1[t], acc21[s]);
-    }
-    EBAR;
-  }
-  s16x8 mb0[4], mb1[4];
-  #pragma unroll
-  for (int t=0;t<4;++t)
-    #pragma unroll
-    for (int j=0;j<8;++j){
-      mb0[t][j] = (short)f2b(silu_f(acc20[(t<<1)+(j>>2)][j&3]));
-      mb1[t][j] = (short)f2b(silu_f(acc21[(t<<1)+(j>>2)][j&3]));
-    }
-  f32x4 acc30[8], acc31[8];
-  #pragma unroll
-  for (int s=0;s<8;++s)
-    #pragma unroll
-    for (int r=0;r<4;++r){
-      const float b = sm.bc1[(s<<4)+(q<<2)+r];
-      acc30[s][r] = b; acc31[s][r] = b;
-    }
-  #pragma unroll
-  for (int t=0;t<4;++t){
-    if (t < 3){ STAGE(13+t); WAITV2; } else { WAITV0; }
-    BARF;
-    #pragma unroll
-    for (int s=0;s<8;++s){
-      const s16x8 A = *(const s16x8*)(&sm.wbuf[t&1][(s<<10)+toff]);
-      acc30[s] = MFMA(A, mb0[t], acc30[s]);
-      acc31[s] = MFMA(A, mb1[t], acc31[s]);
-    }
-    EBAR;
-  }
-
-  float e00=0.f,e01=0.f,e02=0.f, e10=0.f,e11=0.f,e12=0.f;
-  #pragma unroll
-  for (int s=0;s<8;++s)
-    #pragma unroll
-    for (int r=0;r<4;++r){
-      const int f = (s<<4)+(q<<2)+r;
-      const float ev0 = silu_f(acc30[s][r]);
-      const float ev1 = silu_f(acc31[s][r]);
-      e00 += ev0*sm.wc[0][f]; e01 += ev0*sm.wc[1][f]; e02 += ev0*sm.wc[2][f];
-      e10 += ev1*sm.wc[0][f]; e11 += ev1*sm.wc[1][f]; e12 += ev1*sm.wc[2][f];
-    }
-  e00 += __shfl_xor(e00,16); e00 += __shfl_xor(e00,32);
-  e01 += __shfl_xor(e01,16); e01 += __shfl_xor(e01,32);
-  e02 += __shfl_xor(e02,16); e02 += __shfl_xor(e02,32);
-  e10 += __shfl_xor(e10,16); e10 += __shfl_xor(e10,32);
-  e11 += __shfl_xor(e11,16); e11 += __shfl_xor(e11,32);
-  e12 += __shfl_xor(e12,16); e12 += __shfl_xor(e12,32);
-  if (q < 3){
-    const float v0 = (q==0)?e00:((q==1)?e01:e02);
-    const float v1 = (q==0)?e10:((q==1)?e11:e12);
-    const float bq = bec2[q];
-    atomicAdd(&epsb[(size_t)sm.col[el0]*3 + q], v0 + bq);
-    atomicAdd(&epsb[(size_t)sm.col[el1]*3 + q], v1 + bq);
+  int rn[4], cn[4];
+  #pragma unroll
+  for (int e=0;e<4;++e){
+    const int el = (w<<6) + (e<<4) + (lane&15);
+    rn[e] = sm.row[el]; cn[e] = sm.col[el];
+  }
+  s16x8 BA[4][2], BB[4][2];
+  #pragma unroll
+  for (int e=0;e<4;++e){
+    const int el = (w<<6) + (e<<4) + (lane&15);
+    s16x8 bx = {0,0,0,0,0,0,0,0};
+    if (q == 0){
+      bx[0] = (short)f2b(sm.rel[el][0]);
+      bx[1] = (short)f2b(sm.rel[el][1]);
+      bx[2] = (short)f2b(sm.rel[el][2]);
+      bx[3] = (short)f2b(sm.dist[el]);
+      bx[4] = (short)0x3F80;
+    }
+    BA[e][0] = bx;
+    BA[e][1] = *(const s16x8*)(hb + ((size_t)rn[e]<<7) + q8);
+  }
+  f32x4 acc[4][8] = {};
+
+  BARF;
+  #pragma unroll
+  for (int e=0;e<4;++e){
+    BB[e][0] = *(const s16x8*)(hb + ((size_t)rn[e]<<7) + 32 + q8);
+    BB[e][1] = *(const s16x8*)(hb + ((size_t)rn[e]<<7) + 64 + q8);
+  }
+  PH2(0, BA[e][ti], acc);
+  EBAR; STG2(4,0);
+  BARF;
+  #pragma unroll
+  for (int e=0;e<4;++e){
+    BA[e][0] = *(const s16x8*)(hb + ((size_t)rn[e]<<7) + 96 + q8);
+    BA[e][1] = *(const s16x8*)(hb + ((size_t)cn[e]<<7) + q8);
+  }
+  PH2(1, BB[e][ti], acc);
+  EBAR; STG2(6,1);
+  WAITV(12); BARF;
+  #pragma unroll
+  for (int e=0;e<4;++e){
+    BB[e][0] = *(const s16x8*)(hb + ((size_t)cn[e]<<7) + 32 + q8);
+    BB[e][1] = *(const s16x8*)(hb + ((size_t)cn[e]<<7) + 64 + q8);
+  }
+  PH2(0, BA[e][ti], acc);
+  EBAR; STG1(8,0);
+  WAITV(10); BARF;
+  #pragma unroll
+  for (int e=0;e<4;++e)
+    BA[e][0] = *(const s16x8*)(hb + ((size_t)cn[e]<<7) + 96 + q8);
+  PH2(1, BB[e][ti], acc);
+  EBAR; STG2(9,1);
+  WAITV(8); BARF;
+  PH1(0, BA[e][0], acc);
+  EBAR; STG2(11,0);
+
+  s16x8 sb[4][4];
+  #pragma unroll
+  for (int e=0;e<4;++e)
+    #pragma unroll
+    for (int c=0;c<4;++c) sb[e][c] = siluPack(acc[e][2*c], acc[e][2*c+1]);
+  f32x4 acc2[4][8];
+  #pragma unroll
+  for (int s=0;s<8;++s){
+    const f32x4 b = *(const f32x4*)&sm.b2[(s<<4)+(q<<2)];
+    #pragma unroll
+    for (int e=0;e<4;++e) acc2[e][s] = b;
+  }
+  WAITV(4); BARF;
+  PH2(1, sb[e][ti], acc2);
+  EBAR; STG2(13,1);
+  WAITV(4); BARF;
+  PH2(0, sb[e][2+ti], acc2);
+  EBAR; STG2(15,0);
+
+  s16x8 mb[4][4];
+  #pragma unroll
+  for (int e=0;e<4;++e)
+    #pragma unroll
+    for (int c=0;c<4;++c) mb[e][c] = siluPack(acc2[e][2*c], acc2[e][2*c+1]);
+  f32x4 acc3[4][8];
+  #pragma unroll
+  for (int s=0;s<8;++s){
+    const f32x4 b = *(const f32x4*)&sm.bc1[(s<<4)+(q<<2)];
+    #pragma unroll
+    for (int e=0;e<4;++e) acc3[e][s] = b;
+  }
+  WAITV(4); BARF;
+  PH2(1, mb[e][ti], acc3);
+  EBAR;
+  WAITV(0); BARF;
+  PH2(0, mb[e][2+ti], acc3);
+
+  float d0[4]={0,0,0,0}, d1[4]={0,0,0,0}, d2[4]={0,0,0,0};
+  #pragma unroll
+  for (int s=0;s<8;++s){
+    const f32x4 w0 = *(const f32x4*)&sm.wc[0][(s<<4)+(q<<2)];
+    const f32x4 w1 = *(const f32x4*)&sm.wc[1][(s<<4)+(q<<2)];
+    const f32x4 w2 = *(const f32x4*)&sm.wc[2][(s<<4)+(q<<2)];
+    #pragma unroll
+    for (int e=0;e<4;++e)
+      #pragma unroll
+      for (int r=0;r<4;++r){
+        const float ev = silu_f(acc3[e][s][r]);
+        d0[e] += ev*w0[r]; d1[e] += ev*w1[r]; d2[e] += ev*w2[r];
+      }
+  }
+  #pragma unroll
+  for (int e=0;e<4;++e){
+    d0[e] += __shfl_xor(d0[e],16); d0[e] += __shfl_xor(d0[e],32);
+    d1[e] += __shfl_xor(d1[e],16); d1[e] += __shfl_xor(d1[e],32);
+    d2[e] += __shfl_xor(d2[e],16); d2[e] += __shfl_xor(d2[e],32);
+    if (q < 3){
+      const float val = (q==0)?d0[e]:((q==1)?d1[e]:d2[e]);
+      atomicAdd(&epsb[(size_t)cn[e]*3 + q], val + bec2[q]);
+    }
   }
 }
 
@@ -766,15 +777,15 @@
     Wn2T[i] = (unsigned short*)alloc((size_t)128*128*2);
   }
   unsigned short* Wh1T  = (unsigned short*)alloc((size_t)128*128*2);
-  unsigned short* blobL = (unsigned short*)alloc((size_t)NLAYERS*65536*2);
-  unsigned short* blobE = (unsigned short*)alloc((size_t)65536*2);
+  unsigned short* blobL = (unsigned short*)alloc((size_t)NLAYERS*17*4096*2);
+  unsigned short* blobE = (unsigned short*)alloc((size_t)17*4096*2);
   unsigned short* hb    = (unsigned short*)alloc((size_t)N_NODES*HDIM*2);
   int* degi   = (int*)alloc((size_t)N_NODES*4);
   int* offv   = (int*)alloc((size_t)N_NODES*4);
   int* cursor = (int*)alloc((size_t)N_NODES*4);
   int* bsum   = (int*)alloc(4096);
   float* cu   = (float*)alloc((size_t)N_NODES*3*4);
-  int* elist  = (int*)alloc((size_t)N_EDGES*4);
+  int* perm   = (int*)alloc((size_t)N_EDGES*4);
   char* big   = alloc((size_t)N_EDGES*HDIM*2);
   const bool use_csr = ((size_t)(wp - (char*)d_ws) <= ws_size);
   unsigned short* m_buf = (unsigned short*)big;
@@ -790,11 +801,15 @@
     conv(Wn2 + (size_t)i*128*128, Wn2T[i], 7);
   }
   conv(Wh1,  Wh1T,  7);
-  for (int i=0;i<NLAYERS;++i)
-    k_conv_blob<<<dim3(256), dim3(256), 0, stream>>>(
-        Wm1 + (size_t)i*257*128, Wm2 + (size_t)i*128*128, Wc1 + (size_t)i*128*128,
-        blobL + (size_t)i*65536);
-  k_conv_blob<<<dim3(256), dim3(256), 0, stream>>>(Wem1, Wem2, Wec1, blobE);
+  const int cb_grid = (17*4096)/256;
+  for (int i=0;i<NLAYERS;++i){
+    const float* Wm1i = Wm1 + (size_t)i*257*128;
+    k_conv_blob<<<dim3(cb_grid), dim3(256), 0, stream>>>(
+        Wm1i, Wm2 + (size_t)i*128*128, Wc1 + (size_t)i*128*128,
+        Wm1i + (size_t)256*128, bm1 + i*128, 1, blobL + (size_t)i*17*4096);
+  }
+  k_conv_blob<<<dim3(cb_grid), dim3(256), 0, stream>>>(
+      Wem1, Wem2, Wec1, Wem1 + (size_t)256*128, bem1, 4, blobE);
 
   hipMemsetAsync(degi, 0, (size_t)N_NODES*4, stream);
   k_degree<<<dim3((N_EDGES+255)/256), dim3(256), 0, stream>>>(coli, degi);
@@ -803,7 +818,7 @@
     k_scanA<<<dim3(nb), dim3(256), 0, stream>>>(degi, offv, bsum);
     k_scanB<<<dim3(1), dim3(256), 0, stream>>>(bsum, nb);
     k_scanC<<<dim3(nb), dim3(256), 0, stream>>>(offv, bsum, cursor);
-    k_fill<<<dim3((N_EDGES+255)/256), dim3(256), 0, stream>>>(coli, cursor, elist);
+    k_fill<<<dim3((N_EDGES+255)/256), dim3(256), 0, stream>>>(coli, cursor, perm);
   }
   k_xcopy<<<dim3((N_NODES*3+255)/256), dim3(256), 0, stream>>>(x_in, xbuf);
   k_embed<<<dim3((N_NODES+63)/64), dim3(256), 0, stream>>>(h_in, WembT, b_emb, hbuf, hb);
@@ -811,29 +826,26 @@
   for (int i=0;i<NLAYERS;++i){
     hipMemsetAsync(cu, 0, (size_t)N_NODES*3*4, stream);
     if (!use_csr) hipMemsetAsync(agg, 0, (size_t)N_NODES*HDIM*4, stream);
-    const float* wm1r256 = Wm1 + (size_t)i*257*128 + (size_t)256*128;
+    const unsigned short* blob_i = blobL + (size_t)i*17*4096;
     if (use_csr){
-      k_edge_mlp<true><<<dim3(N_EDGES/128), dim3(256), 0, stream>>>(
-        hb, xbuf, rowi, coli, blobL + (size_t)i*65536,
-        bm1 + i*128, wm1r256, bm2 + i*128, bc1 + i*128, Wc2 + i*128,
-        m_buf, agg, cu);
+      k_edge_mlp<true><<<dim3(N_EDGES/256), dim3(256), 0, stream>>>(
+        hb, xbuf, rowi, coli, perm, blob_i,
+        bm2 + i*128, bc1 + i*128, Wc2 + i*128, m_buf, agg, cu);
       k_node_mlp<true><<<dim3((N_NODES+63)/64), dim3(256), 0, stream>>>(
-        hbuf, hb, xbuf, m_buf, agg, offv, degi, elist, cu,
+        hbuf, hb, xbuf, m_buf, agg, offv, degi, cu,
         Wn1T[i], bn1 + i*128, Wn2T[i], bn2 + i*128, lng + i*128, lnb + i*128);
     } else {
-      k_edge_mlp<false><<<dim3(N_EDGES/128), dim3(256), 0, stream>>>(
-        hb, xbuf, rowi, coli, blobL + (size_t)i*65536,
-        bm1 + i*128, wm1r256, bm2 + i*128, bc1 + i*128, Wc2 + i*128,
-        m_buf, agg, cu);
+      k_edge_mlp<false><<<dim3(N_EDGES/256), dim3(256), 0, stream>>>(
+        hb, xbuf, rowi, coli, perm, blob_i,
+        bm2 + i*128, bc1 + i*128, Wc2 + i*128, m_buf, agg, cu);
       k_node_mlp<false><<<dim3((N_NODES+63)/64), dim3(256), 0, stream>>>(
-        hbuf, hb, xbuf, m_buf, agg, offv, degi, elist, cu,
+        hbuf, hb, xbuf, m_buf, agg, offv, degi, cu,
         Wn1T[i], bn1 + i*128, Wn2T[i], bn2 + i*128, lng + i*128, lnb + i*128);
     }
   }
   hipMemsetAsync(epsb, 0, (size_t)N_NODES*3*4, stream);
-  k_eps_edge<<<dim3(N_EDGES/128), dim3(256), 0, stream>>>(
-    hb, xbuf, rowi, coli, blobE,
-    bem1, Wem1 + (size_t)256*128, bem2, bec1, Wec2, bec2, epsb);
+  k_eps_edge<<<dim3(N_EDGES/256), dim3(256), 0, stream>>>(
+    hb, xbuf, rowi, coli, blobE, bem2, bec1, Wec2, bec2, epsb);
   k_eps_node<<<dim3((N_NODES+63)/64), dim3(256), 0, stream>>>(
     hbuf, xbuf, Wh1T, bh1, Wh1 + (size_t)128*128, Wh2, bh2, epsb);
 }
```

New measurement: 1.264 ms. 1.09x faster.
